# Kernel tuning notes

Measured on AMD Instinct MI355X. Metric: run time of the kernel, lower is better.

The kernel has to match this reference:

```python
import jax, jax.numpy as jnp
import numpy as np

C = 64          # channels
K = 7           # 19 - 6*num with num=2 (conv_first, avg_pool, snake kernel size)
GN_GROUPS = C // 4


def conv2d(x, w, b=None, pad=(0, 0), groups=1):
    out = jax.lax.conv_general_dilated(
        x, w, window_strides=(1, 1),
        padding=((pad[0], pad[0]), (pad[1], pad[1])),
        dimension_numbers=('NCHW', 'OIHW', 'NCHW'),
        feature_group_count=groups)
    if b is not None:
        out = out + b[None, :, None, None]
    return out


def avg_pool(x, k, pad):
    # torch AvgPool2d default count_include_pad=True -> always divide by k*k
    s = jax.lax.reduce_window(x, 0.0, jax.lax.add, (1, 1, k, k), (1, 1, 1, 1),
                              ((0, 0), (0, 0), (pad, pad), (pad, pad)))
    return s / float(k * k)


def bn_eval(x, g, b, m, v, eps):
    inv = g / jnp.sqrt(v + eps)
    return x * inv[None, :, None, None] + (b - m * inv)[None, :, None, None]


def group_norm(x, g, b, groups, eps=1e-5):
    B, Ch, H, W = x.shape
    xr = x.reshape(B, groups, Ch // groups, H, W)
    mu = xr.mean(axis=(2, 3, 4), keepdims=True)
    var = xr.var(axis=(2, 3, 4), keepdims=True)
    xr = (xr - mu) / jnp.sqrt(var + eps)
    return xr.reshape(B, Ch, H, W) * g[None, :, None, None] + b[None, :, None, None]


def cum_offset(off):
    # Faithful to DSCNet DSC: center point pinned to 0, offsets accumulate outward
    # via `for index in range(1, center)`. The two endpoints keep their RAW,
    # DETACHED offsets (original code's off-by-one quirk on the detached clone).
    k = off.shape[1]
    c = k // 2
    new = [None] * k
    new[c] = jnp.zeros_like(off[:, c])
    for i in range(1, c):
        new[c + i] = new[c + i - 1] + off[:, c + i]
        new[c - i] = new[c - i + 1] + off[:, c - i]
    new[0] = jax.lax.stop_gradient(off[:, 0])
    new[k - 1] = jax.lax.stop_gradient(off[:, k - 1])
    return jnp.stack(new, axis=1)


def bilinear(feat, y, x):
    # feat [B,C,R,Cc]; y,x [B,K,R,Cc] -> samples [B,C,K,R,Cc]
    B, Ch, R, Cc = feat.shape
    y0 = jnp.floor(y)
    x0 = jnp.floor(x)
    y0i = jnp.clip(y0.astype(jnp.int32), 0, R - 1)
    y1i = jnp.clip(y0.astype(jnp.int32) + 1, 0, R - 1)
    x0i = jnp.clip(x0.astype(jnp.int32), 0, Cc - 1)
    x1i = jnp.clip(x0.astype(jnp.int32) + 1, 0, Cc - 1)
    gather = jax.vmap(lambda f, yi, xi: f[:, yi, xi])  # [C,R,Cc],[K,R,Cc]->[C,K,R,Cc]
    va0 = gather(feat, y0i, x0i)
    vc0 = gather(feat, y0i, x1i)
    va1 = gather(feat, y1i, x0i)
    vc1 = gather(feat, y1i, x1i)
    # interpolation weights use coords clamped to [0, max+1] (faithful to original)
    y0f = jnp.clip(y0, 0.0, float(R))
    y1f = jnp.clip(y0 + 1.0, 0.0, float(R))
    x0f = jnp.clip(x0, 0.0, float(Cc))
    x1f = jnp.clip(x0 + 1.0, 0.0, float(Cc))
    wa0 = ((y1f - y) * (x1f - x))[:, None]
    wc0 = ((y1f - y) * (x - x0f))[:, None]
    wa1 = ((y - y0f) * (x1f - x))[:, None]
    wc1 = ((y - y0f) * (x - x0f))[:, None]
    return va0 * wa0 + vc0 * wc0 + va1 * wa1 + vc1 * wc1


def dsconv(x, off_w, off_b, bn_g, bn_b, bn_m, bn_v, dsc_w, dsc_b, gn_g, gn_b, morph):
    # Dynamic Snake Conv (extend_scope=1, if_offset=True)
    B, Ch, R, Cc = x.shape
    off = jnp.tanh(bn_eval(conv2d(x, off_w, off_b, (1, 1)), bn_g, bn_b, bn_m, bn_v, 1e-5))
    y_off, x_off = off[:, :K], off[:, K:]
    spread = (jnp.arange(K, dtype=x.dtype) - K // 2)[None, :, None, None]
    rows = jnp.arange(R, dtype=x.dtype)[None, None, :, None]
    cols = jnp.arange(Cc, dtype=x.dtype)[None, None, None, :]
    if morph == 0:  # kernel spreads along x, snake swings in y
        y = rows + cum_offset(y_off)
        xc = cols + spread
    else:           # kernel spreads along y, snake swings in x
        y = rows + spread
        xc = cols + cum_offset(x_off)
    y = jnp.broadcast_to(y, (B, K, R, Cc))
    xc = jnp.broadcast_to(xc, (B, K, R, Cc))
    samp = bilinear(x, y, xc)  # [B,C,K,R,Cc]
    # strided (K,1)/(1,K) conv over the deformed map == contraction over (in, k)
    out = jnp.einsum('oik,bikrc->borc', dsc_w, samp) + dsc_b[None, :, None, None]
    out = group_norm(out, gn_g, gn_b, GN_GROUPS)
    return jax.nn.relu(out)


def setup_inputs() -> dict:
    key = jax.random.key(0)
    kit = iter(jax.random.split(key, 64))

    def rn(shape):
        if len(shape) == 1:
            return jax.random.normal(next(kit), shape, jnp.float32) * 0.05
        fan_in = int(np.prod(shape[1:]))
        return jax.random.normal(next(kit), shape, jnp.float32) / np.sqrt(fan_in)

    B, H, W = 2, 192, 192
    d = {}
    d['x'] = jax.random.normal(next(kit), (B, C, H, W), jnp.float32)
    d['w_first'] = rn((C, C, K, K))
    d['hc1_w'] = rn((C, 1, 1, 9)); d['hc1_b'] = rn((C,))
    d['hc2_w'] = rn((C, 1, 1, 7)); d['hc2_b'] = rn((C,))
    d['hc3_w'] = rn((C, 1, 1, 5)); d['hc3_b'] = rn((C,))
    d['vc1_w'] = rn((C, 1, 9, 1)); d['vc1_b'] = rn((C,))
    d['vc2_w'] = rn((C, 1, 7, 1)); d['vc2_b'] = rn((C,))
    d['vc3_w'] = rn((C, 1, 5, 1)); d['vc3_b'] = rn((C,))
    for p in ('h', 'v'):
        d[p + '_off_w'] = rn((2 * K, C, 3, 3)); d[p + '_off_b'] = rn((2 * K,))
        d[p + '_bn_g'] = 1.0 + rn((2 * K,)); d[p + '_bn_b'] = rn((2 * K,))
        d[p + '_bn_m'] = rn((2 * K,))
        d[p + '_bn_v'] = jax.random.uniform(next(kit), (2 * K,), jnp.float32) + 0.5
        d[p + '_dsc_w'] = rn((C, C, K)); d[p + '_dsc_b'] = rn((C,))
        d[p + '_gn_g'] = 1.0 + rn((C,)); d[p + '_gn_b'] = rn((C,))
    d['last_w'] = rn((C, C, 1, 1))
    d['last_g'] = 1.0 + rn((C,)); d['last_b'] = rn((C,))
    d['last_m'] = rn((C,))
    d['last_v'] = jax.random.uniform(next(kit), (C,), jnp.float32) + 0.5
    return d


def reference(x, w_first, hc1_w, hc1_b, hc2_w, hc2_b, hc3_w, hc3_b,
              vc1_w, vc1_b, vc2_w, vc2_b, vc3_w, vc3_b,
              h_off_w, h_off_b, h_bn_g, h_bn_b, h_bn_m, h_bn_v,
              h_dsc_w, h_dsc_b, h_gn_g, h_gn_b,
              v_off_w, v_off_b, v_bn_g, v_bn_b, v_bn_m, v_bn_v,
              v_dsc_w, v_dsc_b, v_gn_g, v_gn_b,
              last_w, last_g, last_b, last_m, last_v):
    x1 = avg_pool(conv2d(x, w_first, None, (K // 2, K // 2)), K, K // 2)
    h = conv2d(x1, hc1_w, hc1_b, (0, 4), groups=C)
    h = conv2d(h, hc2_w, hc2_b, (0, 3), groups=C)
    h = conv2d(h, hc3_w, hc3_b, (0, 2), groups=C)
    h = dsconv(h, h_off_w, h_off_b, h_bn_g, h_bn_b, h_bn_m, h_bn_v,
               h_dsc_w, h_dsc_b, h_gn_g, h_gn_b, morph=0)
    v = conv2d(x1, vc1_w, vc1_b, (4, 0), groups=C)
    v = conv2d(v, vc2_w, vc2_b, (3, 0), groups=C)
    v = conv2d(v, vc3_w, vc3_b, (2, 0), groups=C)
    v = dsconv(v, v_off_w, v_off_b, v_bn_g, v_bn_b, v_bn_m, v_bn_v,
               v_dsc_w, v_dsc_b, v_gn_g, v_gn_b, morph=1)
    out = h + v + x1
    out = conv2d(out, last_w, None, (0, 0))          # 1x1, bias=False (norm present)
    out = bn_eval(out, last_g, last_b, last_m, last_v, 1e-3)
    return out * jax.nn.sigmoid(out)                  # SiLU
```

## Files before the change

kernel.cpp:

```cpp
#include <hip/hip_runtime.h>
#include <hip/hip_bf16.h>
#include <hip/hip_fp16.h>
#include <math.h>

#define Bq 2
#define Cq 64
#define Hq 192
#define Wq 192
#define HWq (Hq*Wq)
#define Nq ((size_t)Bq*Cq*HWq)

typedef __attribute__((ext_vector_type(8))) _Float16 f16x8;
typedef __attribute__((ext_vector_type(4))) float f32x4;

__device__ inline unsigned short h2us(__half h) {
  union { __half h; unsigned short u; } v; v.h = h; return v.u;
}

__global__ __launch_bounds__(256) void prep_all_kernel(
    const float* hc1_w, const float* hc1_b, const float* hc2_w, const float* hc2_b,
    const float* hc3_w, const float* hc3_b,
    const float* vc1_w, const float* vc1_b, const float* vc2_w, const float* vc2_b,
    const float* vc3_w, const float* vc3_b,
    const float* h_off_w, const float* h_off_b, const float* h_bn_g, const float* h_bn_b,
    const float* h_bn_m, const float* h_bn_v,
    const float* v_off_w, const float* v_off_b, const float* v_bn_g, const float* v_bn_b,
    const float* v_bn_m, const float* v_bn_v,
    const float* last_w, const float* last_g, const float* last_b, const float* last_m,
    const float* last_v,
    const float* __restrict__ w_first,
    const float* __restrict__ h_dsc_w, const float* __restrict__ v_dsc_w,
    float* wEffH, float* bEffH, float* wEffV, float* bEffV,
    float* wOffH, float* bOffH, float* wOffV, float* bOffV,
    float* lwT, float* lbO, float* wB,
    unsigned short* __restrict__ wtpH, unsigned short* __restrict__ wtpV,
    unsigned short* __restrict__ wpack)
{
  int bid = blockIdx.x;
  int t = threadIdx.x;
  if (bid == 0) {
    if (t < 128) {
      int ch = t & 63;
      bool ish = t < 64;
      const float* w1p = (ish ? hc1_w : vc1_w) + ch*9;
      const float* w2p = (ish ? hc2_w : vc2_w) + ch*7;
      const float* w3p = (ish ? hc3_w : vc3_w) + ch*5;
      float w1r[9], w2r[7], w3r[5];
#pragma unroll
      for (int j = 0; j < 9; j++) w1r[j] = w1p[j];
#pragma unroll
      for (int k = 0; k < 7; k++) w2r[k] = w2p[k];
#pragma unroll
      for (int m = 0; m < 5; m++) w3r[m] = w3p[m];
      float t15[15];
#pragma unroll
      for (int s = 0; s < 15; s++) {
        float a = 0.f;
#pragma unroll
        for (int j = 0; j < 9; j++) { int k2 = s - j; if (k2 >= 0 && k2 < 7) a += w1r[j]*w2r[k2]; }
        t15[s] = a;
      }
      float* we = (ish ? wEffH : wEffV) + ch*19;
#pragma unroll
      for (int s = 0; s < 19; s++) {
        float a = 0.f;
#pragma unroll
        for (int j = 0; j < 15; j++) { int k3 = s - j; if (k3 >= 0 && k3 < 5) a += t15[j]*w3r[k3]; }
        we[s] = a;
      }
      float S2 = 0.f, S3 = 0.f;
#pragma unroll
      for (int j = 0; j < 7; j++) S2 += w2r[j];
#pragma unroll
      for (int j = 0; j < 5; j++) S3 += w3r[j];
      float b1 = (ish ? hc1_b : vc1_b)[ch];
      float b2 = (ish ? hc2_b : vc2_b)[ch];
      float b3 = (ish ? hc3_b : vc3_b)[ch];
      (ish ? bEffH : bEffV)[ch] = b1*S2*S3 + b2*S3 + b3;
    }
    for (int idx = t; idx < 9*64*7; idx += 256) {
      int tap = idx / 448; int rem = idx % 448; int i = rem / 7; int m = rem % 7;
      float invh = h_bn_g[m] / sqrtf(h_bn_v[m] + 1e-5f);
      wOffH[(tap*64 + i)*8 + m] = h_off_w[(m*64 + i)*9 + tap] * invh;
      float invv = v_bn_g[7+m] / sqrtf(v_bn_v[7+m] + 1e-5f);
      wOffV[(tap*64 + i)*8 + m] = v_off_w[((7+m)*64 + i)*9 + tap] * invv;
    }
    if (t < 7) {
      float invh = h_bn_g[t] / sqrtf(h_bn_v[t] + 1e-5f);
      bOffH[t] = h_off_b[t]*invh + h_bn_b[t] - h_bn_m[t]*invh;
      float invv = v_bn_g[7+t] / sqrtf(v_bn_v[7+t] + 1e-5f);
      bOffV[t] = v_off_b[7+t]*invv + v_bn_b[7+t] - v_bn_m[7+t]*invv;
    }
    for (int idx = t; idx < 4096; idx += 256) {
      int o = idx % 64; int i = idx / 64;
      float inv = last_g[o] / sqrtf(last_v[o] + 1e-3f);
      lwT[i*64 + o] = last_w[o*64 + i] * inv;
    }
    if (t < 64) {
      float inv = last_g[t] / sqrtf(last_v[t] + 1e-3f);
      lbO[t] = last_b[t] - last_m[t]*inv;
    }
  } else if (bid <= 9) {
    int tid = (bid - 1)*256 + t;
    if (tid >= 2*64*18) return;
    int cls = tid % 18;
    int ch  = (tid / 18) % 64;
    int br  = tid / (18*64);
    int c = (cls < 9) ? cls : cls + 174;
    const float* w1p = (br==0 ? hc1_w : vc1_w) + ch*9;
    const float* w2p = (br==0 ? hc2_w : vc2_w) + ch*7;
    const float* w3p = (br==0 ? hc3_w : vc3_w) + ch*5;
    float b1 = (br==0 ? hc1_b : vc1_b)[ch];
    float b2 = (br==0 ? hc2_b : vc2_b)[ch];
    float b3 = (br==0 ? hc3_b : vc3_b)[ch];
    float w1r[9], w2r[7], w3r[5];
#pragma unroll
    for (int j = 0; j < 9; j++) w1r[j] = w1p[j];
#pragma unroll
    for (int k = 0; k < 7; k++) w2r[k] = w2p[k];
#pragma unroll
    for (int m = 0; m < 5; m++) w3r[m] = w3p[m];
    float acc[19];
#pragma unroll
    for (int s = 0; s < 19; s++) acc[s] = 0.f;
    float bacc = b3;
#pragma unroll
    for (int m = 0; m < 5; m++) {
      int d = c + m - 2;
      bool dok = (d >= 0 && d < Wq);
      float s2b = b2;
#pragma unroll
      for (int k = 0; k < 7; k++) {
        int e = d + k - 3;
        bool eok = (e >= 0 && e < Wq);
        if (eok) s2b += w2r[k] * b1;
        float wmk = w3r[m] * w2r[k];
#pragma unroll
        for (int j = 0; j < 9; j++) {
          int fd = e + j - 4;
          bool fok = (fd >= 0 && fd < Wq);
          float contrib = (dok && eok && fok) ? wmk * w1r[j] : 0.f;
          acc[m + k + j] += contrib;
        }
      }
      if (dok) bacc += w3r[m] * s2b;
    }
    float* dst = wB + ((size_t)(br*64 + ch)*18 + cls)*20;
#pragma unroll
    for (int s = 0; s < 19; s++) dst[s] = acc[s];
    dst[19] = bacc;
  } else {
    int tid = (bid - 10)*256 + t;
    int nthr = 64*256;
    for (int idx = tid; idx < 7*2*2*64*32; idx += nthr) {
      int ch32 = idx & 31;
      int oc   = (idx >> 5) & 63;
      int hl   = (idx >> 11) & 1;
      int kc   = (idx >> 12) & 1;
      int tap  = idx >> 13;
      int i = kc*32 + ch32;
      float vh = h_dsc_w[oc*448 + i*7 + tap];
      float vv = v_dsc_w[oc*448 + i*7 + tap];
      _Float16 hh = (_Float16)vh;
      _Float16 hv = (_Float16)vv;
      unsigned short uh, uv;
      if (!hl) { uh = *(unsigned short*)&hh; uv = *(unsigned short*)&hv; }
      else {
        _Float16 lh = (_Float16)(vh - (float)hh);
        _Float16 lv = (_Float16)(vv - (float)hv);
        uh = *(unsigned short*)&lh; uv = *(unsigned short*)&lv;
      }
      wtpH[idx] = uh; wtpV[idx] = uv;
    }
    for (int e = tid; e < 2*49*2*64*32; e += nthr) {
      int ch  = e & 31;
      int oc  = (e >> 5) & 63;
      int hl  = (e >> 11) & 1;
      int rest = e >> 12;
      int tap = rest % 49;
      int h   = rest / 49;
      float wv = w_first[((size_t)oc*64 + h*32 + ch)*49 + tap];
      __half hh = __float2half(wv);
      unsigned short us;
      if (!hl) us = h2us(hh);
      else { float rr = wv - __half2float(hh); us = h2us(__float2half(rr)); }
      wpack[e] = us;
    }
  }
}

__global__ __launch_bounds__(192) void tof16_pack_kernel(const float* __restrict__ x,
                                                         unsigned short* __restrict__ xpack)
{
  __shared__ unsigned int s[192*64];
  int r = blockIdx.x, b = blockIdx.y;
  int t = threadIdx.x;
  for (int ch = 0; ch < 64; ch++) {
    float v = x[((size_t)(b*64+ch)*Hq + r)*Wq + t];
    _Float16 hh = (_Float16)v;
    s[t*64 + (ch ^ (t & 31))] = (unsigned int)*(unsigned short*)&hh;
  }
  __syncthreads();
  unsigned short* dst = xpack + ((size_t)b*Hq + r)*Wq*64;
  for (int i = 0; i < 8; i++) {
    int gidx = i*192 + t;
    int c = gidx >> 3, g = gidx & 7;
    unsigned short tmp[8];
#pragma unroll
    for (int j = 0; j < 8; j++) {
      int ch = g*8 + j;
      tmp[j] = (unsigned short)s[c*64 + (ch ^ (c & 31))];
    }
    uint4 v;
    v.x = (unsigned int)tmp[0] | ((unsigned int)tmp[1] << 16);
    v.y = (unsigned int)tmp[2] | ((unsigned int)tmp[3] << 16);
    v.z = (unsigned int)tmp[4] | ((unsigned int)tmp[5] << 16);
    v.w = (unsigned int)tmp[6] | ((unsigned int)tmp[7] << 16);
    *(uint4*)(dst + (size_t)gidx*8) = v;
  }
}

__global__ __launch_bounds__(256) void conv7_mfma_kernel(
    const unsigned short* __restrict__ xpack,
    const unsigned short* __restrict__ wpack,
    float* __restrict__ out)
{
  __shared__ __align__(16) unsigned short sA[8*54*32];
  int ct = blockIdx.x;
  int rt = blockIdx.y;
  int b  = blockIdx.z;
  int r0 = rt*2, c0 = ct*48;
  int t = threadIdx.x;
  int wv = t >> 6;
  int l  = t & 63;
  int l15 = l & 15, lg = l >> 4;
  int oc = wv*16 + l15;

  f32x4 acc[2][3];
#pragma unroll
  for (int i = 0; i < 2; i++)
#pragma unroll
    for (int j = 0; j < 3; j++) acc[i][j] = (f32x4){0.f,0.f,0.f,0.f};

  for (int h = 0; h < 2; h++) {
    __syncthreads();
    for (int idx = t; idx < 8*54*4; idx += 256) {
      int g = idx & 3, pix = idx >> 2;
      int row = pix / 54, col = pix % 54;
      int gr = r0 - 3 + row, gc = c0 - 3 + col;
      uint4 v = {0u,0u,0u,0u};
      if (gr >= 0 && gr < Hq && gc >= 0 && gc < Wq)
        v = *(const uint4*)(xpack + (((size_t)b*Hq + gr)*Wq + gc)*64 + (h*4 + g)*8);
      ((uint4*)sA)[(row*54 + col)*4 + (g ^ ((col >> 1) & 3))] = v;
    }
    __syncthreads();
    const unsigned short* wb = wpack + (size_t)h*49*4096;
#pragma unroll 7
    for (int tap = 0; tap < 49; tap++) {
      int dy = tap / 7, dx = tap % 7;
      f16x8 bh = *(const f16x8*)(wb + (size_t)tap*4096 +        oc*32 + lg*8);
      f16x8 bl = *(const f16x8*)(wb + (size_t)tap*4096 + 2048 + oc*32 + lg*8);
#pragma unroll
      for (int rw = 0; rw < 2; rw++) {
        int arow = rw + dy;
        f16x8 a[3];
#pragma unroll
        for (int tc = 0; tc < 3; tc++) {
          int col = tc*16 + l15 + dx;
          a[tc] = *(const f16x8*)((const uint4*)sA + (arow*54 + col)*4 + (lg ^ ((col >> 1) & 3)));
        }
#pragma unroll
        for (int tc = 0; tc < 3; tc++) {
          acc[rw][tc] = __builtin_amdgcn_mfma_f32_16x16x32_f16(a[tc], bh, acc[rw][tc], 0, 0, 0);
          acc[rw][tc] = __builtin_amdgcn_mfma_f32_16x16x32_f16(a[tc], bl, acc[rw][tc], 0, 0, 0);
        }
      }
    }
  }
#pragma unroll
  for (int rw = 0; rw < 2; rw++) {
    float* dst = out + ((size_t)(b*64 + oc)*Hq + (r0 + rw))*Wq + c0;
#pragma unroll
    for (int tc = 0; tc < 3; tc++) {
      f32x4 v = acc[rw][tc];
      *(float4*)(dst + tc*16 + lg*4) = make_float4(v[0], v[1], v[2], v[3]);
    }
  }
}

__global__ __launch_bounds__(256) void pool_fused_kernel(const float* __restrict__ in,
                                                         float* __restrict__ out)
{
  __shared__ float raw[38][192];
  __shared__ float cs[32][192];
  int rt = blockIdx.x;
  int plane = blockIdx.y;
  int r0 = rt*32;
  int t = threadIdx.x;
  const float* src = in + (size_t)plane*HWq;
  for (int idx = t; idx < 38*192; idx += 256) {
    int lr = idx / 192, c = idx % 192;
    int gr = r0 - 3 + lr;
    raw[lr][c] = (gr >= 0 && gr < Hq) ? src[gr*Wq + c] : 0.f;
  }
  __syncthreads();
  for (int idx = t; idx < 32*192; idx += 256) {
    int lr = idx / 192, c = idx % 192;
    float s = 0.f;
#pragma unroll
    for (int dr = 0; dr < 7; dr++) s += raw[lr + dr][c];
    cs[lr][c] = s;
  }
  __syncthreads();
  float* dst = out + (size_t)plane*HWq + r0*Wq;
  for (int idx = t; idx < 32*192; idx += 256) {
    int lr = idx / 192, c = idx % 192;
    float s = 0.f;
#pragma unroll
    for (int dc = -3; dc <= 3; dc++) {
      int cc = c + dc;
      if (cc >= 0 && cc < Wq) s += cs[lr][cc];
    }
    dst[idx] = s * (1.f/49.f);
  }
}

__global__ __launch_bounds__(256) void dwf_kernel(const float* __restrict__ x1,
                                                  const float* __restrict__ wEffH,
                                                  const float* __restrict__ bEffH,
                                                  const float* __restrict__ wBH,
                                                  const float* __restrict__ wEffV,
                                                  const float* __restrict__ bEffV,
                                                  const float* __restrict__ wBV,
                                                  unsigned short* __restrict__ packH,
                                                  unsigned short* __restrict__ packV)
{
  __shared__ float sW[8][19][20];
  int z = blockIdx.z;
  int br = z >> 1, b = z & 1;
  const float* wEff = br ? wEffV : wEffH;
  const float* bEff = br ? bEffV : bEffH;
  const float* wB   = br ? wBV   : wBH;
  unsigned short* pack = br ? packV : packH;
  int g8 = blockIdx.y;
  int t = threadIdx.x;
  int chb = g8*8;
  for (int i = t; i < 8*380; i += 256) {
    int ch8 = i / 380; int rem = i % 380;
    int row = rem / 20, jj = rem % 20;
    int ch = chb + ch8;
    float v;
    if (row < 18) v = wB[((size_t)ch*18 + row)*20 + jj];
    else v = (jj < 19) ? wEff[ch*19 + jj] : bEff[ch];
    sW[ch8][row][jj] = v;
  }
  __syncthreads();
  int p = blockIdx.x*256 + t;
  int r = p / Wq, c = p % Wq;
  float vals[8];
  if (br == 0) {
    int row = (c < 9) ? c : ((c >= Wq-9) ? (c - 174) : 18);
#pragma unroll
    for (int ch8 = 0; ch8 < 8; ch8++) {
      const float* src = x1 + (size_t)(b*Cq + chb + ch8)*HWq + r*Wq;
      float s = sW[ch8][row][19];
#pragma unroll
      for (int j = 0; j < 19; j++) {
        int idx = min(max(c + j - 9, 0), Wq-1);
        s += src[idx] * sW[ch8][row][j];
      }
      vals[ch8] = s;
    }
  } else {
    int row = (r < 9) ? r : ((r >= Hq-9) ? (r - 174) : 18);
#pragma unroll
    for (int ch8 = 0; ch8 < 8; ch8++) {
      const float* src = x1 + (size_t)(b*Cq + chb + ch8)*HWq + c;
      float s = sW[ch8][row][19];
#pragma unroll
      for (int j = 0; j < 19; j++) {
        int idx = min(max(r + j - 9, 0), Hq-1);
        s += src[idx*Wq] * sW[ch8][row][j];
      }
      vals[ch8] = s;
    }
  }
  unsigned int hi[4], lo[4];
#pragma unroll
  for (int q = 0; q < 4; q++) {
    __half h0 = __float2half(vals[2*q]);
    __half h1 = __float2half(vals[2*q+1]);
    __half l0 = __float2half(vals[2*q]   - __half2float(h0));
    __half l1 = __float2half(vals[2*q+1] - __half2float(h1));
    hi[q] = (unsigned int)h2us(h0) | ((unsigned int)h2us(h1) << 16);
    lo[q] = (unsigned int)h2us(l0) | ((unsigned int)h2us(l1) << 16);
  }
  *(uint4*)(pack + (((size_t)b*16 + g8)*HWq + p)*8)     = make_uint4(hi[0], hi[1], hi[2], hi[3]);
  *(uint4*)(pack + (((size_t)b*16 + 8 + g8)*HWq + p)*8) = make_uint4(lo[0], lo[1], lo[2], lo[3]);
}

__global__ __launch_bounds__(256) void off_cum_kernel(const unsigned short* __restrict__ fpH,
                                                      const unsigned short* __restrict__ fpV,
                                                      const float* __restrict__ wOffH,
                                                      const float* __restrict__ bOffH,
                                                      const float* __restrict__ wOffV,
                                                      const float* __restrict__ bOffV,
                                                      float* __restrict__ hcum,
                                                      float* __restrict__ vcum)
{
  const size_t HW8 = (size_t)HWq*8;
  int bid = blockIdx.x;
  int xcd = bid & 7, lid = bid >> 3;
  int combo = xcd >> 1;
  int br = combo >> 1, b = combo & 1;
  int pxblk = (xcd & 1)*72 + lid;
  const unsigned short* fp = br ? fpV : fpH;
  const float* wOff = br ? wOffV : wOffH;
  const float* bOff = br ? bOffV : bOffH;
  float* cum = br ? vcum : hcum;
  int p = pxblk*256 + threadIdx.x;
  int r = p / Wq, c = p % Wq;
  float tv[7];
#pragma unroll
  for (int m = 0; m < 7; m++) tv[m] = bOff[m];
  const unsigned short* fb = fp + (size_t)b*HWq*128;
  for (int tap = 0; tap < 9; tap++) {
    int dy = tap/3 - 1, dx = tap%3 - 1;
    int rr = r + dy, cc = c + dx;
    if (rr < 0 || rr >= Hq || cc < 0 || cc >= Wq) continue;
    const unsigned short* p0 = fb + ((size_t)rr*Wq + cc)*8;
    const float* wp = wOff + tap*512;
    for (int g = 0; g < 8; g++) {
      f16x8 hv = *(const f16x8*)(p0 + (size_t)g*HW8);
      f16x8 lv = *(const f16x8*)(p0 + (size_t)(8 + g)*HW8);
#pragma unroll
      for (int e = 0; e < 8; e++) {
        float fv = (float)hv[e] + (float)lv[e];
        const float* wr = wp + (g*8 + e)*8;
#pragma unroll
        for (int m = 0; m < 7; m++) tv[m] += fv * wr[m];
      }
    }
  }
#pragma unroll
  for (int m = 0; m < 7; m++) tv[m] = tanhf(tv[m]);
  float c0 = tv[0], c1 = tv[1] + tv[2], c2 = tv[2], c3 = 0.f;
  float c4 = tv[4], c5 = tv[4] + tv[5], c6 = tv[6];
  size_t bb = (size_t)b*7*HWq + p;
  cum[bb + 0*HWq] = c0; cum[bb + 1*HWq] = c1; cum[bb + 2*HWq] = c2;
  cum[bb + 3*HWq] = c3; cum[bb + 4*HWq] = c4; cum[bb + 5*HWq] = c5;
  cum[bb + 6*HWq] = c6;
}

__global__ __launch_bounds__(64, 3) void einsum_mfma_kernel(
    const unsigned short* __restrict__ fpH, const unsigned short* __restrict__ fpV,
    const float* __restrict__ cumH, const float* __restrict__ cumV,
    const unsigned short* __restrict__ wtpHp, const unsigned short* __restrict__ wtpVp,
    const float* __restrict__ dscbH, const float* __restrict__ dscbV,
    float* __restrict__ outH, float* __restrict__ outV,
    float* __restrict__ pstat)
{
  __shared__ __align__(16) unsigned short sA[2*32*64];
  const size_t HW8 = (size_t)HWq*8;
  int morph = blockIdx.y;
  const unsigned short* fp  = morph ? fpV   : fpH;
  const float* cum          = morph ? cumV  : cumH;
  const unsigned short* wtp = morph ? wtpVp : wtpHp;
  const float* dsc_b        = morph ? dscbV : dscbH;
  float* out                = morph ? outV  : outH;
  int bid = blockIdx.x;
  int swz = (bid & 7)*288 + (bid >> 3);
  int b   = swz / 1152;
  int blk = swz % 1152;
  int l = threadIdx.x;
  int l15 = l & 15, lg = l >> 4;
  int l7 = l & 7;
  int px5 = l & 31;
  int chh = l >> 5;
  int p = blk*32 + px5;
  int r = p / Wq, c = p % Wq;

  int fixc   = morph ? r : c;
  int vbase  = morph ? c : r;
  int stride = morph ? 1 : Wq;

  f32x4 acc[2][4];
#pragma unroll
  for (int i = 0; i < 2; i++)
#pragma unroll
    for (int j = 0; j < 4; j++) acc[i][j] = (f32x4){0.f,0.f,0.f,0.f};

  const unsigned short* fb = fp + (size_t)b*HWq*128;

  f16x8 a0r[4], a1r[4];
  float w0, w1;
  bool oob;

#define ISSUE(KK)                                                           \
  {                                                                         \
    int fx = fixc + (KK) - 3;                                               \
    oob = (fx < 0 || fx >= 192);                                            \
    float vf = (float)vbase + cum[((size_t)(b*7 + (KK)))*HWq + p];          \
    float v0 = floorf(vf);                                                  \
    int v0q = (int)v0;                                                      \
    int v0i = min(max(v0q, 0), 191);                                        \
    int v1i = min(max(v0q + 1, 0), 191);                                    \
    float v0f = fminf(fmaxf(v0, 0.f), 192.f);                               \
    float v1f = fminf(fmaxf(v0 + 1.f, 0.f), 192.f);                         \
    w0 = v1f - vf; w1 = vf - v0f;                                           \
    int fixoff = morph ? fx*Wq : fx;                                        \
    const unsigned short* p0 = fb + (size_t)(fixoff + v0i*stride)*8;        \
    const unsigned short* p1 = fb + (size_t)(fixoff + v1i*stride)*8;        \
    if (!oob) {                                                             \
      _Pragma("unroll")                                                     \
      for (int gi = 0; gi < 4; gi++) {                                      \
        int g = chh*4 + gi;                                                 \
        a0r[gi] = *(const f16x8*)(p0 + (size_t)g*HW8);                      \
        a1r[gi] = *(const f16x8*)(p1 + (size_t)g*HW8);                      \
      }                                                                     \
    }                                                                       \
  }

#define WRITE(SLOT)                                                         \
  {                                                                         \
    unsigned short* myrow = sA + (size_t)((SLOT)*32 + px5)*64;              \
    if (oob) {                                                              \
      uint4 z = {0u,0u,0u,0u};                                              \
      _Pragma("unroll")                                                     \
      for (int gi = 0; gi < 4; gi++)                                        \
        *(uint4*)(myrow + (size_t)(((chh*4 + gi) ^ l7))*8) = z;             \
    } else {                                                                \
      _Pragma("unroll")                                                     \
      for (int gi = 0; gi < 4; gi++) {                                      \
        f16x8 sh;                                                           \
        _Pragma("unroll")                                                   \
        for (int e = 0; e < 8; e++) {                                       \
          float v = w0*(float)a0r[gi][e] + w1*(float)a1r[gi][e];            \
          sh[e] = (_Float16)v;                                              \
        }                                                                   \
        *(f16x8*)(myrow + (size_t)(((chh*4 + gi) ^ l7))*8) = sh;            \
      }                                                                     \
    }                                                                       \
  }

#define MFMA_TAP(KK, SLOT)                                                  \
  {                                                                         \
    _Pragma("unroll")                                                       \
    for (int kc = 0; kc < 2; kc++) {                                        \
      const unsigned short* wbase = wtp + (size_t)(((KK)*2 + kc)*2)*2048;   \
      f16x8 bh[4], bl[4];                                                   \
      _Pragma("unroll")                                                     \
      for (int tb = 0; tb < 4; tb++) {                                      \
        bh[tb] = *(const f16x8*)(wbase + (tb*16 + l15)*32 + lg*8);          \
        bl[tb] = *(const f16x8*)(wbase + 2048 + (tb*16 + l15)*32 + lg*8);   \
      }                                                                     \
      f16x8 ah[2];                                                          \
      _Pragma("unroll")                                                     \
      for (int ta = 0; ta < 2; ta++) {                                      \
        const unsigned short* rbase = sA + (size_t)((SLOT)*32 + ta*16 + l15)*64; \
        ah[ta] = *(const f16x8*)(rbase + (size_t)((kc*4 + lg) ^ l7)*8);     \
      }                                                                     \
      _Pragma("unroll")                                                     \
      for (int ta = 0; ta < 2; ta++)                                        \
        _Pragma("unroll")                                                   \
        for (int tb = 0; tb < 4; tb++) {                                    \
          acc[ta][tb] = __builtin_amdgcn_mfma_f32_16x16x32_f16(ah[ta], bh[tb], acc[ta][tb], 0, 0, 0); \
          acc[ta][tb] = __builtin_amdgcn_mfma_f32_16x16x32_f16(ah[ta], bl[tb], acc[ta][tb], 0, 0, 0); \
        }                                                                   \
    }                                                                       \
  }

  ISSUE(0);
  WRITE(0);
#pragma unroll 1
  for (int k = 0; k < 7; k++) {
    int slot = k & 1;
    if (k < 6) ISSUE(k+1);
    MFMA_TAP(k, slot);
    if (k < 6) WRITE((k+1) & 1);
  }
#undef ISSUE
#undef WRITE
#undef MFMA_TAP

  int pbase = blk*32;
#pragma unroll
  for (int tb = 0; tb < 4; tb++) {
    int oc = tb*16 + l15;
    float bias = dsc_b[oc];
    float* dst = out + (size_t)(b*64 + oc)*HWq + pbase;
    float s = 0.f, ss = 0.f;
#pragma unroll
    for (int ta = 0; ta < 2; ta++) {
      f32x4 v = acc[ta][tb];
      float v0 = v[0]+bias, v1 = v[1]+bias, v2 = v[2]+bias, v3 = v[3]+bias;
      *(float4*)(dst + ta*16 + lg*4) = make_float4(v0, v1, v2, v3);
      s  += v0 + v1 + v2 + v3;
      ss += v0*v0 + v1*v1 + v2*v2 + v3*v3;
    }
    s  += __shfl_xor(s, 16);
    s  += __shfl_xor(s, 32);
    ss += __shfl_xor(ss, 16);
    ss += __shfl_xor(ss, 32);
    if (lg == 0) {
      float* pp = pstat + ((size_t)(morph*2304 + swz))*128 + oc*2;
      pp[0] = s; pp[1] = ss;
    }
  }
}

__global__ __launch_bounds__(256) void gnred_kernel(const float* __restrict__ pstat,
                                                    float* __restrict__ stats)
{
  int combo = blockIdx.x;
  int buf = combo >> 7;
  int rem = combo & 127;
  int b = rem >> 6, ch = rem & 63;
  int t = threadIdx.x;
  float s = 0.f, ss = 0.f;
  for (int q = t; q < 1152; q += 256) {
    const float* pp = pstat + ((size_t)(buf*2304 + b*1152 + q))*128 + ch*2;
    s += pp[0]; ss += pp[1];
  }
  __shared__ float red[2][4];
  for (int off = 32; off; off >>= 1) {
    s  += __shfl_down(s, off);
    ss += __shfl_down(ss, off);
  }
  if ((t & 63) == 0) { red[0][t >> 6] = s; red[1][t >> 6] = ss; }
  __syncthreads();
  if (t == 0) {
    s  = red[0][0] + red[0][1] + red[0][2] + red[0][3];
    ss = red[1][0] + red[1][1] + red[1][2] + red[1][3];
    stats[combo*2 + 0] = s;
    stats[combo*2 + 1] = ss;
  }
}

__global__ __launch_bounds__(256) void gnfinal_kernel(const float* __restrict__ stats,
                                                      const float* __restrict__ h_gn_g, const float* __restrict__ h_gn_b,
                                                      const float* __restrict__ v_gn_g, const float* __restrict__ v_gn_b,
                                                      float* __restrict__ gnAB)
{
  int t = threadIdx.x;
  int buf = t >> 7, ch = t & 63;
  int base = t & ~3;
  float sum = 0.f, ss = 0.f;
#pragma unroll
  for (int q = 0; q < 4; q++) { sum += stats[(base+q)*2]; ss += stats[(base+q)*2 + 1]; }
  const float n = 4.f * HWq;
  float mean = sum / n;
  float var = ss / n - mean*mean;
  float gg = (buf ? v_gn_g : h_gn_g)[ch];
  float bb = (buf ? v_gn_b : h_gn_b)[ch];
  float A = gg / sqrtf(var + 1e-5f);
  gnAB[t*2 + 0] = A;
  gnAB[t*2 + 1] = bb - mean*A;
}

__global__ __launch_bounds__(256) void final2_kernel(const float* __restrict__ hbuf,
                                                     const float* __restrict__ vbuf,
                                                     const float* __restrict__ x1,
                                                     const float* __restrict__ gnAB,
                                                     const float* __restrict__ lwT,
                                                     const float* __restrict__ lbO,
                                                     float* __restrict__ out)
{
  int b = blockIdx.y;
  int p = blockIdx.x*256 + threadIdx.x;
  float acc[64];
#pragma unroll
  for (int o = 0; o < 64; o++) acc[o] = 0.f;
  for (int i = 0; i < 64; i++) {
    size_t off = (size_t)(b*64 + i)*HWq + p;
    int plane = b*64 + i;
    int ih = plane*2;
    int iv = (128 + plane)*2;
    float hv = fmaxf(hbuf[off]*gnAB[ih] + gnAB[ih+1], 0.f);
    float vv = fmaxf(vbuf[off]*gnAB[iv] + gnAB[iv+1], 0.f);
    float cv = hv + vv + x1[off];
    const float* wr = lwT + i*64;
#pragma unroll
    for (int o = 0; o < 64; o++) acc[o] += cv * wr[o];
  }
  float* dst = out + (size_t)b*Cq*HWq + p;
#pragma unroll
  for (int o = 0; o < 64; o++) {
    float yv = acc[o] + lbO[o];
    dst[(size_t)o*HWq] = yv / (1.f + expf(-yv));
  }
}

extern "C" void kernel_launch(void* const* d_in, const int* in_sizes, int n_in,
                              void* d_out, int out_size, void* d_ws, size_t ws_size,
                              hipStream_t stream)
{
  const float* x       = (const float*)d_in[0];
  const float* w_first = (const float*)d_in[1];
  float* ws = (float*)d_ws;

  float* bufA = ws;
  float* bufB = ws + Nq;
  float* x1   = ws + 2*Nq;
  float* h_ds = ws + 3*Nq;
  float* v_ds = ws + 4*Nq;
  size_t off = 5*Nq;
  float* hcum  = ws + off; off += (size_t)Bq*7*HWq;
  float* vcum  = ws + off; off += (size_t)Bq*7*HWq;
  float* wEffH = ws + off; off += 64*19;
  float* bEffH = ws + off; off += 64;
  float* wEffV = ws + off; off += 64*19;
  float* bEffV = ws + off; off += 64;
  float* wtH   = ws + off; off += 64*64*7;
  float* wtV   = ws + off; off += 64*64*7;
  float* wOffH = ws + off; off += 9*64*8;
  float* bOffH = ws + off; off += 8;
  float* wOffV = ws + off; off += 9*64*8;
  float* bOffV = ws + off; off += 8;
  float* lwT   = ws + off; off += 64*64;
  float* lbO   = ws + off; off += 64;
  float* stats = ws + off; off += 512;
  float* gnAB  = ws + off; off += 512;
  float* wB    = ws + off; off += 2*64*18*20;
  float* pstat = ws + off; off += (size_t)2*2304*128;
  unsigned short* wpack = (unsigned short*)(ws + off); off += 2*49*2*64*32/2 + 16;
  unsigned short* xpack  = (unsigned short*)h_ds;
  unsigned short* fpackH = (unsigned short*)h_ds;
  unsigned short* fpackV = (unsigned short*)v_ds;
  unsigned short* wtpH = (unsigned short*)wtH;
  unsigned short* wtpV = (unsigned short*)wtV;

  prep_all_kernel<<<dim3(74), dim3(256), 0, stream>>>(
      (const float*)d_in[2],  (const float*)d_in[3],  (const float*)d_in[4],  (const float*)d_in[5],
      (const float*)d_in[6],  (const float*)d_in[7],
      (const float*)d_in[8],  (const float*)d_in[9],  (const float*)d_in[10], (const float*)d_in[11],
      (const float*)d_in[12], (const float*)d_in[13],
      (const float*)d_in[14], (const float*)d_in[15], (const float*)d_in[16], (const float*)d_in[17],
      (const float*)d_in[18], (const float*)d_in[19],
      (const float*)d_in[24], (const float*)d_in[25], (const float*)d_in[26], (const float*)d_in[27],
      (const float*)d_in[28], (const float*)d_in[29],
      (const float*)d_in[34], (const float*)d_in[35], (const float*)d_in[36], (const float*)d_in[37],
      (const float*)d_in[38],
      w_first, (const float*)d_in[20], (const float*)d_in[30],
      wEffH, bEffH, wEffV, bEffV, wOffH, bOffH, wOffV, bOffV, lwT, lbO, wB,
      wtpH, wtpV, wpack);

  tof16_pack_kernel<<<dim3(Hq, Bq), dim3(192), 0, stream>>>(x, xpack);
  conv7_mfma_kernel<<<dim3(4, 96, 2), dim3(256), 0, stream>>>(xpack, wpack, bufA);

  pool_fused_kernel<<<dim3(6, 128), dim3(256), 0, stream>>>(bufA, x1);

  dwf_kernel<<<dim3(144, 8, 4), dim3(256), 0, stream>>>(x1, wEffH, bEffH, wB,
      wEffV, bEffV, wB + 64*18*20, fpackH, fpackV);

  off_cum_kernel<<<dim3(576), dim3(256), 0, stream>>>(fpackH, fpackV,
      wOffH, bOffH, wOffV, bOffV, hcum, vcum);

  einsum_mfma_kernel<<<dim3(2304, 2), dim3(64), 0, stream>>>(fpackH, fpackV,
      hcum, vcum, wtpH, wtpV, (const float*)d_in[21], (const float*)d_in[31], bufA, bufB, pstat);

  gnred_kernel<<<dim3(256), dim3(256), 0, stream>>>(pstat, stats);
  gnfinal_kernel<<<dim3(1), dim3(256), 0, stream>>>(stats,
      (const float*)d_in[22], (const float*)d_in[23],
      (const float*)d_in[32], (const float*)d_in[33], gnAB);

  final2_kernel<<<dim3(144, 2), dim3(256), 0, stream>>>(bufA, bufB, x1, gnAB, lwT, lbO, (float*)d_out);
}
```

Measured before the change: 304.5 us.

## Compute offset conv with MFMA using split fp16 hi/lo weights

Rewrites the 3x3 offset convolution (64->7 channels) as an MFMA 16x16x32 f16 GEMM per tap. Weights are prepacked in the prep kernel as hi/lo fp16 pairs, padded to 16 output columns, and three MFMAs (hh, hl, lh) recover near-fp32 accuracy. Each 64-thread block now handles 32 pixels. The tanh and cumulative-offset step uses lane shuffles instead of per-thread scalar FMAs. This targets the scalar FMA and weight-load cost of the old per-pixel loop, at the price of wasted MFMA columns from padding 7 outputs to 16 and scattered 4-element output stores.

After: 283.5 us. 1.07x faster.

```diff
diff --git a/kernel.cpp b/kernel.cpp
--- a/kernel.cpp
+++ b/kernel.cpp
@@ -31,7 +31,8 @@
     const float* __restrict__ w_first,
     const float* __restrict__ h_dsc_w, const float* __restrict__ v_dsc_w,
     float* wEffH, float* bEffH, float* wEffV, float* bEffV,
-    float* wOffH, float* bOffH, float* wOffV, float* bOffV,
+    unsigned short* __restrict__ wOpH, unsigned short* __restrict__ wOpV,
+    float* bOffH, float* bOffV,
     float* lwT, float* lbO, float* wB,
     unsigned short* __restrict__ wtpH, unsigned short* __restrict__ wtpV,
     unsigned short* __restrict__ wpack)
@@ -78,12 +79,30 @@
       float b3 = (ish ? hc3_b : vc3_b)[ch];
       (ish ? bEffH : bEffV)[ch] = b1*S2*S3 + b2*S3 + b3;
     }
-    for (int idx = t; idx < 9*64*7; idx += 256) {
-      int tap = idx / 448; int rem = idx % 448; int i = rem / 7; int m = rem % 7;
-      float invh = h_bn_g[m] / sqrtf(h_bn_v[m] + 1e-5f);
-      wOffH[(tap*64 + i)*8 + m] = h_off_w[(m*64 + i)*9 + tap] * invh;
-      float invv = v_bn_g[7+m] / sqrtf(v_bn_v[7+m] + 1e-5f);
-      wOffV[(tap*64 + i)*8 + m] = v_off_w[((7+m)*64 + i)*9 + tap] * invv;
+    for (int idx = t; idx < 9*2*2*16*32; idx += 256) {
+      int k  = idx & 31;
+      int n  = (idx >> 5) & 15;
+      int hl = (idx >> 9) & 1;
+      int kc = (idx >> 10) & 1;
+      int tap = idx >> 11;
+      int ch = kc*32 + k;
+      float wh = 0.f, wv2 = 0.f;
+      if (n < 7) {
+        float invh = h_bn_g[n] / sqrtf(h_bn_v[n] + 1e-5f);
+        wh = h_off_w[((size_t)n*64 + ch)*9 + tap] * invh;
+        float invv = v_bn_g[7+n] / sqrtf(v_bn_v[7+n] + 1e-5f);
+        wv2 = v_off_w[((size_t)(7+n)*64 + ch)*9 + tap] * invv;
+      }
+      _Float16 hh = (_Float16)wh;
+      _Float16 hv = (_Float16)wv2;
+      unsigned short uh, uv;
+      if (!hl) { uh = *(unsigned short*)&hh; uv = *(unsigned short*)&hv; }
+      else {
+        _Float16 lh = (_Float16)(wh - (float)hh);
+        _Float16 lv = (_Float16)(wv2 - (float)hv);
+        uh = *(unsigned short*)&lh; uv = *(unsigned short*)&lv;
+      }
+      wOpH[idx] = uh; wOpV[idx] = uv;
     }
     if (t < 7) {
       float invh = h_bn_g[t] / sqrtf(h_bn_v[t] + 1e-5f);
@@ -399,57 +418,102 @@
   *(uint4*)(pack + (((size_t)b*16 + 8 + g8)*HWq + p)*8) = make_uint4(lo[0], lo[1], lo[2], lo[3]);
 }
 
-__global__ __launch_bounds__(256) void off_cum_kernel(const unsigned short* __restrict__ fpH,
-                                                      const unsigned short* __restrict__ fpV,
-                                                      const float* __restrict__ wOffH,
-                                                      const float* __restrict__ bOffH,
-                                                      const float* __restrict__ wOffV,
-                                                      const float* __restrict__ bOffV,
-                                                      float* __restrict__ hcum,
-                                                      float* __restrict__ vcum)
+__global__ __launch_bounds__(64, 4) void off_cum_kernel(
+    const unsigned short* __restrict__ fpH, const unsigned short* __restrict__ fpV,
+    const unsigned short* __restrict__ wOpH, const unsigned short* __restrict__ wOpV,
+    const float* __restrict__ bOffH, const float* __restrict__ bOffV,
+    float* __restrict__ hcum, float* __restrict__ vcum)
 {
   const size_t HW8 = (size_t)HWq*8;
   int bid = blockIdx.x;
   int xcd = bid & 7, lid = bid >> 3;
   int combo = xcd >> 1;
   int br = combo >> 1, b = combo & 1;
-  int pxblk = (xcd & 1)*72 + lid;
-  const unsigned short* fp = br ? fpV : fpH;
-  const float* wOff = br ? wOffV : wOffH;
+  int wv = (xcd & 1)*576 + lid;
+  const unsigned short* fp  = br ? fpV  : fpH;
+  const unsigned short* wOp = br ? wOpV : wOpH;
   const float* bOff = br ? bOffV : bOffH;
   float* cum = br ? vcum : hcum;
-  int p = pxblk*256 + threadIdx.x;
-  int r = p / Wq, c = p % Wq;
-  float tv[7];
-#pragma unroll
-  for (int m = 0; m < 7; m++) tv[m] = bOff[m];
+  int pb = wv*32;
+  int l = threadIdx.x;
+  int l15 = l & 15, lg = l >> 4;
   const unsigned short* fb = fp + (size_t)b*HWq*128;
+
+  int r0[2], c0[2];
+#pragma unroll
+  for (int ta = 0; ta < 2; ta++) {
+    int px = pb + ta*16 + l15;
+    r0[ta] = px / Wq; c0[ta] = px % Wq;
+  }
+
+  f32x4 acc[2];
+  acc[0] = (f32x4){0.f,0.f,0.f,0.f};
+  acc[1] = (f32x4){0.f,0.f,0.f,0.f};
+
+#pragma unroll 1
   for (int tap = 0; tap < 9; tap++) {
     int dy = tap/3 - 1, dx = tap%3 - 1;
-    int rr = r + dy, cc = c + dx;
-    if (rr < 0 || rr >= Hq || cc < 0 || cc >= Wq) continue;
-    const unsigned short* p0 = fb + ((size_t)rr*Wq + cc)*8;
-    const float* wp = wOff + tap*512;
-    for (int g = 0; g < 8; g++) {
-      f16x8 hv = *(const f16x8*)(p0 + (size_t)g*HW8);
-      f16x8 lv = *(const f16x8*)(p0 + (size_t)(8 + g)*HW8);
-#pragma unroll
-      for (int e = 0; e < 8; e++) {
-        float fv = (float)hv[e] + (float)lv[e];
-        const float* wr = wp + (g*8 + e)*8;
-#pragma unroll
-        for (int m = 0; m < 7; m++) tv[m] += fv * wr[m];
-      }
-    }
-  }
-#pragma unroll
-  for (int m = 0; m < 7; m++) tv[m] = tanhf(tv[m]);
-  float c0 = tv[0], c1 = tv[1] + tv[2], c2 = tv[2], c3 = 0.f;
-  float c4 = tv[4], c5 = tv[4] + tv[5], c6 = tv[6];
-  size_t bb = (size_t)b*7*HWq + p;
-  cum[bb + 0*HWq] = c0; cum[bb + 1*HWq] = c1; cum[bb + 2*HWq] = c2;
-  cum[bb + 3*HWq] = c3; cum[bb + 4*HWq] = c4; cum[bb + 5*HWq] = c5;
-  cum[bb + 6*HWq] = c6;
+    f16x8 Ahi[2][2], Alo[2][2];
+#pragma unroll
+    for (int ta = 0; ta < 2; ta++) {
+      int rr = r0[ta] + dy, cc = c0[ta] + dx;
+      bool ok = (rr >= 0 && rr < Hq && cc >= 0 && cc < Wq);
+      if (ok) {
+        size_t base = (size_t)(rr*Wq + cc)*8;
+#pragma unroll
+        for (int kc = 0; kc < 2; kc++) {
+          int g = kc*4 + lg;
+          const unsigned short* p0 = fb + (size_t)g*HW8 + base;
+          Ahi[ta][kc] = *(const f16x8*)p0;
+          Alo[ta][kc] = *(const f16x8*)(p0 + (size_t)8*HW8);
+        }
+      } else {
+        uint4 z = {0u,0u,0u,0u};
+#pragma unroll
+        for (int kc = 0; kc < 2; kc++) {
+          *(uint4*)&Ahi[ta][kc] = z;
+          *(uint4*)&Alo[ta][kc] = z;
+        }
+      }
+    }
+    f16x8 Bh[2], Bl[2];
+#pragma unroll
+    for (int kc = 0; kc < 2; kc++) {
+      const unsigned short* wb = wOp + (size_t)((tap*2 + kc)*2)*512 + l15*32 + lg*8;
+      Bh[kc] = *(const f16x8*)wb;
+      Bl[kc] = *(const f16x8*)(wb + 512);
+    }
+#pragma unroll
+    for (int ta = 0; ta < 2; ta++)
+#pragma unroll
+      for (int kc = 0; kc < 2; kc++) {
+        acc[ta] = __builtin_amdgcn_mfma_f32_16x16x32_f16(Ahi[ta][kc], Bh[kc], acc[ta], 0, 0, 0);
+        acc[ta] = __builtin_amdgcn_mfma_f32_16x16x32_f16(Ahi[ta][kc], Bl[kc], acc[ta], 0, 0, 0);
+        acc[ta] = __builtin_amdgcn_mfma_f32_16x16x32_f16(Alo[ta][kc], Bh[kc], acc[ta], 0, 0, 0);
+      }
+  }
+
+  float bias = (l15 < 7) ? bOff[l15] : 0.f;
+  size_t cb = (size_t)b*7*HWq;
+  int src_up = (l & 48) | ((l15 + 1) & 15);
+  int src_dn = (l & 48) | ((l15 - 1) & 15);
+#pragma unroll
+  for (int ta = 0; ta < 2; ta++) {
+    int pxb = pb + ta*16 + lg*4;
+#pragma unroll
+    for (int j = 0; j < 4; j++) {
+      float v = tanhf(acc[ta][j] + bias);
+      float vup = __shfl(v, src_up);
+      float vdn = __shfl(v, src_dn);
+      if (l15 < 7) {
+        float o = v;
+        if (l15 == 1) o += vup;
+        if (l15 == 5) o += vdn;
+        if (l15 == 3) o = 0.f;
+        cum[cb + (size_t)l15*HWq + pxb + j] = o;
+      }
+    }
+  }
 }
 
 __global__ __launch_bounds__(64, 3) void einsum_mfma_kernel(
@@ -713,9 +777,9 @@
   float* bEffV = ws + off; off += 64;
   float* wtH   = ws + off; off += 64*64*7;
   float* wtV   = ws + off; off += 64*64*7;
-  float* wOffH = ws + off; off += 9*64*8;
+  float* wOpHf = ws + off; off += 9216;
+  float* wOpVf = ws + off; off += 9216;
   float* bOffH = ws + off; off += 8;
-  float* wOffV = ws + off; off += 9*64*8;
   float* bOffV = ws + off; off += 8;
   float* lwT   = ws + off; off += 64*64;
   float* lbO   = ws + off; off += 64;
@@ -729,6 +793,8 @@
   unsigned short* fpackV = (unsigned short*)v_ds;
   unsigned short* wtpH = (unsigned short*)wtH;
   unsigned short* wtpV = (unsigned short*)wtV;
+  unsigned short* wOpH = (unsigned short*)wOpHf;
+  unsigned short* wOpV = (unsigned short*)wOpVf;
 
   prep_all_kernel<<<dim3(74), dim3(256), 0, stream>>>(
       (const float*)d_in[2],  (const float*)d_in[3],  (const float*)d_in[4],  (const float*)d_in[5],
@@ -742,7 +808,7 @@
       (const float*)d_in[34], (const float*)d_in[35], (const float*)d_in[36], (const float*)d_in[37],
       (const float*)d_in[38],
       w_first, (const float*)d_in[20], (const float*)d_in[30],
-      wEffH, bEffH, wEffV, bEffV, wOffH, bOffH, wOffV, bOffV, lwT, lbO, wB,
+      wEffH, bEffH, wEffV, bEffV, wOpH, wOpV, bOffH, bOffV, lwT, lbO, wB,
       wtpH, wtpV, wpack);
 
   tof16_pack_kernel<<<dim3(Hq, Bq), dim3(192), 0, stream>>>(x, xpack);
@@ -753,8 +819,8 @@
   dwf_kernel<<<dim3(144, 8, 4), dim3(256), 0, stream>>>(x1, wEffH, bEffH, wB,
       wEffV, bEffV, wB + 64*18*20, fpackH, fpackV);
 
-  off_cum_kernel<<<dim3(576), dim3(256), 0, stream>>>(fpackH, fpackV,
-      wOffH, bOffH, wOffV, bOffV, hcum, vcum);
+  off_cum_kernel<<<dim3(4608), dim3(64), 0, stream>>>(fpackH, fpackV,
+      wOpH, wOpV, bOffH, bOffV, hcum, vcum);
 
   einsum_mfma_kernel<<<dim3(2304, 2), dim3(64), 0, stream>>>(fpackH, fpackV,
       hcum, vcum, wtpH, wtpV, (const float*)d_in[21], (const float*)d_in[31], bufA, bufB, pstat);
```
